# Performance work log

Hardware: AMD Instinct MI355X
Metric: run time of the kernel (lower is better)

## Reference

```python
import jax, jax.numpy as jnp
import numpy as np

N, K, H, W = 2048, 8, 128, 128
G = 50              # glimpse size (50x50 from tem_rnn input 50*50)
ENC = 100           # glimpse encoder output (relation_rnn input arithmetic)
HID = 256
D_REL = ENC + (3 + 50) * 2 + HID          # 462
D_TEM = G * G + (3 + 50) * 2 + HID        # 2862


def _lin(k, out_d, in_d, scale=0.02):
    k1, k2 = jax.random.split(k)
    return (jax.random.normal(k1, (out_d, in_d), jnp.float32) * scale,
            jax.random.normal(k2, (out_d,), jnp.float32) * scale)


def _lstm_params(k, in_d, hid):
    k1, k2, k3, k4 = jax.random.split(k, 4)
    s = 0.02
    return (jax.random.normal(k1, (4 * hid, in_d), jnp.float32) * s,
            jax.random.normal(k2, (4 * hid, hid), jnp.float32) * s,
            jax.random.normal(k3, (4 * hid,), jnp.float32) * s,
            jax.random.normal(k4, (4 * hid,), jnp.float32) * s)


def lstm_cell(x, h, c, Wih, Whh, bih, bhh):
    g = x @ Wih.T + h @ Whh.T + (bih + bhh)
    i, f, gg, o = jnp.split(g, 4, axis=-1)
    i, f, o = jax.nn.sigmoid(i), jax.nn.sigmoid(f), jax.nn.sigmoid(o)
    c2 = f * c + i * jnp.tanh(gg)
    return o * jnp.tanh(c2), c2


def _bilinear_one(im, py, px):
    # im [H,W]; py,px [G,G] pixel coords; zeros padding like torch grid_sample
    x0 = jnp.floor(px); y0 = jnp.floor(py)
    wx1 = px - x0; wy1 = py - y0
    x0i = x0.astype(jnp.int32); y0i = y0.astype(jnp.int32)

    def gather(yi, xi):
        valid = (yi >= 0) & (yi < H) & (xi >= 0) & (xi < W)
        v = im[jnp.clip(yi, 0, H - 1), jnp.clip(xi, 0, W - 1)]
        return jnp.where(valid, v, 0.0)

    return ((1 - wy1) * (1 - wx1) * gather(y0i, x0i)
            + (1 - wy1) * wx1 * gather(y0i, x0i + 1)
            + wy1 * (1 - wx1) * gather(y0i + 1, x0i)
            + wy1 * wx1 * gather(y0i + 1, x0i + 1))


def stn_glimpse(z_where, img):
    # z_where [n,3] = (scale, tx, ty); theta = [[s,0,tx],[0,s,ty]] (attentive_stn_encode)
    s, tx, ty = z_where[:, 0], z_where[:, 1], z_where[:, 2]
    lin = jnp.linspace(-1.0, 1.0, G)
    gy, gx = jnp.meshgrid(lin, lin, indexing='ij')           # [G,G]
    px = (s[:, None, None] * gx + tx[:, None, None] + 1.0) * 0.5 * (W - 1)
    py = (s[:, None, None] * gy + ty[:, None, None] + 1.0) * 0.5 * (H - 1)
    out = jax.vmap(_bilinear_one)(img, py, px)               # [n,G,G]
    return out.reshape(out.shape[0], G * G)


def setup_inputs() -> dict:
    key = jax.random.key(0)
    ks = jax.random.split(key, 16)
    inp = {
        'img': jax.random.uniform(ks[0], (N, H, W), jnp.float32),
        'z_what_last': jax.random.normal(ks[1], (N, K, 50), jnp.float32),
        'z_where_last': jax.random.normal(ks[2], (N, K, 3), jnp.float32) * 0.3,
        'z_pres_last': jnp.ones((N, K, 1), jnp.float32),
        'hidden_last': jax.random.normal(ks[3], (N, K, HID), jnp.float32),
    }
    inp['W_loca'], inp['b_loca'] = _lin(ks[4], 3, HID)
    inp['Wg'], inp['bg'] = _lin(ks[5], ENC, G * G)
    (inp['Wih_rel'], inp['Whh_rel'], inp['bih_rel'], inp['bhh_rel']) = _lstm_params(ks[6], D_REL, HID)
    (inp['Wih_tem'], inp['Whh_tem'], inp['bih_tem'], inp['bhh_tem']) = _lstm_params(ks[7], D_TEM, HID)
    inp['Wm_wh'], inp['bm_wh'] = _lin(ks[8], 3, HID + 3)
    inp['Ws_wh'], inp['bs_wh'] = _lin(ks[9], 3, HID + 3)
    inp['Wm_wt'], inp['bm_wt'] = _lin(ks[10], 50, 50 + HID + HID)
    inp['Ws_wt'], inp['bs_wt'] = _lin(ks[11], 50, 50 + HID + HID)
    inp['Wm_pr'], inp['bm_pr'] = _lin(ks[12], 1, 50 + 3 + HID + HID)
    inp['Ws_pr'], inp['bs_pr'] = _lin(ks[13], 1, 50 + 3 + HID + HID)
    return inp


def reference(img, z_what_last, z_where_last, z_pres_last, hidden_last,
              W_loca, b_loca, Wg, bg,
              Wih_rel, Whh_rel, bih_rel, bhh_rel,
              Wih_tem, Whh_tem, bih_tem, bhh_tem,
              Wm_wh, bm_wh, Ws_wh, bs_wh,
              Wm_wt, bm_wt, Ws_wt, bs_wt,
              Wm_pr, bm_pr, Ws_pr, bs_pr):
    n = img.shape[0]

    def step(carry, xs):
        h_r, c_r, pzw, pzwhat = carry
        zwl, zwhatl, zpl, hl = xs   # [n,3],[n,50],[n,1],[n,256]
        # prop_loca: relu(linear(hidden)) + z_where_last
        zwb = jax.nn.relu(hl @ W_loca.T + b_loca) + zwl
        # STN glimpse + encode (bias pass)
        enc = jax.nn.relu(stn_glimpse(zwb, img) @ Wg.T + bg)        # [n,100]
        rin = jnp.concatenate([enc, zwl, pzw, zwhatl, pzwhat, hl], -1)  # [n,462]
        h_r2, c_r2 = lstm_cell(rin, h_r, c_r, Wih_rel, Whh_rel, bih_rel, bhh_rel)
        # z_where: latent predictor mean (eval mode)
        zw = jnp.concatenate([zwl, h_r2], -1) @ Wm_wh.T + bm_wh      # [n,3]
        # second STN glimpse with sampled where
        g2 = stn_glimpse(zw, img)                                    # [n,2500]
        tin = jnp.concatenate([g2, zw, pzw, zwhatl, pzwhat, hl], -1) # [n,2862]
        h_t, c_t = lstm_cell(tin, h_r2, c_r2, Wih_tem, Whh_tem, bih_tem, bhh_tem)
        # z_what mean
        zwhat = jnp.concatenate([zwhatl, h_r2, h_t], -1) @ Wm_wt.T + bm_wt  # [n,50]
        # z_pres: deterministic expectation of Bernoulli(mean*std) * previous pres
        zp_cal = jnp.concatenate([zwhat, zw, h_r2, h_t], -1)
        p = jax.nn.sigmoid(zp_cal @ Wm_pr.T + bm_pr) * jax.nn.sigmoid(zp_cal @ Ws_pr.T + bs_pr)
        zp = p * zpl                                                 # [n,1]
        return (h_r2, c_r2, zw, zwhat), (zwhat, zw, zp, h_t)

    carry0 = (jnp.zeros((n, HID), img.dtype), jnp.zeros((n, HID), img.dtype),
              jnp.zeros((n, 3), img.dtype), jnp.zeros((n, 50), img.dtype))
    xs = (jnp.swapaxes(z_where_last, 0, 1), jnp.swapaxes(z_what_last, 0, 1),
          jnp.swapaxes(z_pres_last, 0, 1), jnp.swapaxes(hidden_last, 0, 1))
    _, (zwhat_s, zw_s, zp_s, ht_s) = jax.lax.scan(step, carry0, xs)
    z_what = jnp.swapaxes(zwhat_s, 0, 1)   # [n,K,50]
    z_where = jnp.swapaxes(zw_s, 0, 1)     # [n,K,3]
    z_pres = jnp.swapaxes(zp_s, 0, 1)      # [n,K,1]
    h_temp = jnp.swapaxes(ht_s, 0, 1)      # [n,K,256]
    return z_what, z_where, z_pres, h_temp
```

## Files before the change

### kernel.cpp

```cpp
#include <hip/hip_runtime.h>
#include <hip/hip_bf16.h>
#include <math.h>

typedef __attribute__((ext_vector_type(8))) short bf16x8;
typedef __attribute__((ext_vector_type(4))) float f32x4;
using bf16 = __hip_bfloat16;

constexpr int NN   = 2048;
constexpr int KO   = 8;
constexpr int IH   = 128, IW = 128;
constexpr int GS   = 50;
constexpr int HIDD = 256;
constexpr int RIN_LD = 768;
constexpr int TIN_LD = 3136;
constexpr int G1_LD  = 2560;

__device__ __forceinline__ float sigm(float x) { return 1.f/(1.f+expf(-x)); }

template<int OUT_BF16, int RELU>
__global__ __launch_bounds__(256, 4) void mfma_gemm(
    const bf16* __restrict__ A, int lda, int Ktot,
    const bf16* __restrict__ Wt, int ldw, int M,
    const float* __restrict__ b1, const float* __restrict__ b2,
    void* __restrict__ Cout, int ldc, int nxb, int Kseg, int sstride)
{
    __shared__ __align__(16) bf16 As[2*4096];
    __shared__ __align__(16) bf16 Bs[2*4096];
    const int b    = blockIdx.x;
    const int xcd  = b & 7;
    const int t    = b >> 3;
    const int n0   = (xcd + 8*(t / nxb))*64;
    const int m0   = (t % nxb)*64;
    const int tid  = threadIdx.x;
    const int w    = tid>>6, lane = tid&63;
    const int wy   = w>>1, wx = w&1;
    const int q    = lane>>4, fr = lane&15;

    const int kbeg = blockIdx.y * Kseg;
    const int kend = min(Ktot, kbeg + Kseg);
    const int nk   = (kend - kbeg) >> 6;

    const int r0   = tid>>3;
    const int csrc = ((tid&7)*8) ^ ((r0&7)<<3);
    const bf16* pa = A + (size_t)(n0 + r0)*lda + kbeg + csrc;
    int wmr0 = m0 + r0;       if (wmr0 > M-1) wmr0 = M-1;
    int wmr1 = m0 + r0 + 32;  if (wmr1 > M-1) wmr1 = M-1;
    const bf16* pb  = Wt + (size_t)wmr0*ldw + kbeg + csrc;
    const bf16* pb1 = Wt + (size_t)wmr1*ldw + kbeg + csrc;

    f32x4 acc[2][2] = {};

    auto stage = [&](int buf, int koff) {
        bf16* la = As + buf*4096 + w*512;
        bf16* lb = Bs + buf*4096 + w*512;
        __builtin_amdgcn_global_load_lds(
            (const __attribute__((address_space(1))) void*)(pa + koff),
            (__attribute__((address_space(3))) void*)la, 16, 0, 0);
        __builtin_amdgcn_global_load_lds(
            (const __attribute__((address_space(1))) void*)(pa + koff + 32*(size_t)lda),
            (__attribute__((address_space(3))) void*)(la + 2048), 16, 0, 0);
        __builtin_amdgcn_global_load_lds(
            (const __attribute__((address_space(1))) void*)(pb + koff),
            (__attribute__((address_space(3))) void*)lb, 16, 0, 0);
        __builtin_amdgcn_global_load_lds(
            (const __attribute__((address_space(1))) void*)(pb1 + koff),
            (__attribute__((address_space(3))) void*)(lb + 2048), 16, 0, 0);
    };

    stage(0, 0);
    __syncthreads();
    int cur = 0;
    for (int kt = 0; kt < nk; ++kt) {
        if (kt + 1 < nk) stage(cur ^ 1, (kt + 1) << 6);
        const bf16* Ab = As + cur*4096;
        const bf16* Bb = Bs + cur*4096;
        bf16x8 av[2][2], bv[2][2];
        #pragma unroll
        for (int i=0;i<2;i++) {
            int r = wy*32 + i*16 + fr;
            int sw = (r&7)<<3, base = r*64;
            av[i][0] = *(const bf16x8*)(Ab + base + ((q*8) ^ sw));
            av[i][1] = *(const bf16x8*)(Ab + base + ((32 + q*8) ^ sw));
        }
        #pragma unroll
        for (int j=0;j<2;j++) {
            int r = wx*32 + j*16 + fr;
            int sw = (r&7)<<3, base = r*64;
            bv[j][0] = *(const bf16x8*)(Bb + base + ((q*8) ^ sw));
            bv[j][1] = *(const bf16x8*)(Bb + base + ((32 + q*8) ^ sw));
        }
        #pragma unroll
        for (int h=0;h<2;h++)
            #pragma unroll
            for (int i=0;i<2;i++)
                #pragma unroll
                for (int j=0;j<2;j++)
                    acc[i][j] = __builtin_amdgcn_mfma_f32_16x16x32_bf16(av[i][h], bv[j][h], acc[i][j], 0, 0, 0);
        __syncthreads();
        cur ^= 1;
    }

    #pragma unroll
    for (int j=0;j<2;j++) {
        int col = m0 + wx*32 + j*16 + fr;
        if (col < M) {
            float bias = 0.f;
            if (blockIdx.y == 0) {
                if (b1) bias += b1[col];
                if (b2) bias += b2[col];
            }
            #pragma unroll
            for (int i=0;i<2;i++) {
                #pragma unroll
                for (int reg=0;reg<4;reg++) {
                    float v = acc[i][j][reg] + bias;
                    if (RELU) v = fmaxf(v, 0.f);
                    size_t idx = (size_t)(n0 + wy*32 + i*16 + q*4 + reg)*ldc + col;
                    if (OUT_BF16) ((bf16*)Cout)[idx] = __float2bfloat16(v);
                    else          ((float*)Cout)[(size_t)blockIdx.y*sstride + idx] = v;
                }
            }
        }
    }
}

__device__ __forceinline__ void glimpse_points_global(const float* __restrict__ im,
                                                      float s, float tx, float ty,
                                                      bf16* __restrict__ drow) {
    const float GXS = 2.0f/49.0f;
    const float txp = tx + 1.0f, typ = ty + 1.0f;
    for (int p2 = threadIdx.x; p2 < 1250; p2 += 256) {
        int i = p2 / 25, j = (p2 - i*25)*2;
        float gy  = fmaf((float)i, GXS, -1.0f);
        float py  = fmaf(s, gy, typ)*63.5f;
        float y0f = floorf(py); float fy = py - y0f; int y0 = (int)y0f;
        float wy0 = ((unsigned)y0     < 128u) ? (1.f - fy) : 0.f;
        float wy1 = ((unsigned)(y0+1) < 128u) ? fy         : 0.f;
        const float* r0 = im + min(max(y0,  0),127)*IW;
        const float* r1 = im + min(max(y0+1,0),127)*IW;
        float gxa = fmaf((float)j, GXS, -1.0f);
        float pxa = fmaf(s, gxa, txp)*63.5f;
        float xa0f = floorf(pxa); float fa = pxa - xa0f; int xa0 = (int)xa0f;
        float wa0 = ((unsigned)xa0     < 128u) ? (1.f - fa) : 0.f;
        float wa1 = ((unsigned)(xa0+1) < 128u) ? fa         : 0.f;
        int xa0c = min(max(xa0,  0),127), xa1c = min(max(xa0+1,0),127);
        float gxb = fmaf((float)(j+1), GXS, -1.0f);
        float pxb = fmaf(s, gxb, txp)*63.5f;
        float xb0f = floorf(pxb); float fb = pxb - xb0f; int xb0 = (int)xb0f;
        float wb0 = ((unsigned)xb0     < 128u) ? (1.f - fb) : 0.f;
        float wb1 = ((unsigned)(xb0+1) < 128u) ? fb         : 0.f;
        int xb0c = min(max(xb0,  0),127), xb1c = min(max(xb0+1,0),127);

        float va = fmaf(wy1, fmaf(wa0, r1[xa0c], wa1*r1[xa1c]),
                   wy0 *     fmaf(wa0, r0[xa0c], wa1*r0[xa1c]));
        float vb = fmaf(wy1, fmaf(wb0, r1[xb0c], wb1*r1[xb1c]),
                   wy0 *     fmaf(wb0, r0[xb0c], wb1*r0[xb1c]));

        bf16 b0 = __float2bfloat16(va), b1 = __float2bfloat16(vb);
        unsigned short u0, u1;
        __builtin_memcpy(&u0, &b0, 2); __builtin_memcpy(&u1, &b1, 2);
        *(unsigned int*)(drow + i*GS + j) = (unsigned)u0 | ((unsigned)u1 << 16);
    }
}

__device__ __forceinline__ void sample_pair_lds(const float* __restrict__ im_s,
                                                float s, float txp, float typ,
                                                int i, int j, bf16* __restrict__ drow) {
    const float GXS = 2.0f/49.0f;
    float gy  = fmaf((float)i, GXS, -1.0f);
    float py  = fmaf(s, gy, typ)*63.5f;
    float y0f = floorf(py); float fy = py - y0f; int y0 = (int)y0f;
    float wy0 = ((unsigned)y0     < 128u) ? (1.f - fy) : 0.f;
    float wy1 = ((unsigned)(y0+1) < 128u) ? fy         : 0.f;
    const float* r0 = im_s + min(max(y0,  0),127)*IW;
    const float* r1 = im_s + min(max(y0+1,0),127)*IW;
    float gxa = fmaf((float)j, GXS, -1.0f);
    float pxa = fmaf(s, gxa, txp)*63.5f;
    float xa0f = floorf(pxa); float fa = pxa - xa0f; int xa0 = (int)xa0f;
    float wa0 = ((unsigned)xa0     < 128u) ? (1.f - fa) : 0.f;
    float wa1 = ((unsigned)(xa0+1) < 128u) ? fa         : 0.f;
    int xa0c = min(max(xa0,  0),127), xa1c = min(max(xa0+1,0),127);
    float gxb = fmaf((float)(j+1), GXS, -1.0f);
    float pxb = fmaf(s, gxb, txp)*63.5f;
    float xb0f = floorf(pxb); float fb = pxb - xb0f; int xb0 = (int)xb0f;
    float wb0 = ((unsigned)xb0     < 128u) ? (1.f - fb) : 0.f;
    float wb1 = ((unsigned)(xb0+1) < 128u) ? fb         : 0.f;
    int xb0c = min(max(xb0,  0),127), xb1c = min(max(xb0+1,0),127);
    float va = fmaf(wy1, fmaf(wa0, r1[xa0c], wa1*r1[xa1c]),
               wy0 *     fmaf(wa0, r0[xa0c], wa1*r0[xa1c]));
    float vb = fmaf(wy1, fmaf(wb0, r1[xb0c], wb1*r1[xb1c]),
               wy0 *     fmaf(wb0, r0[xb0c], wb1*r0[xb1c]));
    bf16 b0 = __float2bfloat16(va), b1 = __float2bfloat16(vb);
    unsigned short u0, u1;
    __builtin_memcpy(&u0, &b0, 2); __builtin_memcpy(&u1, &b1, 2);
    *(unsigned int*)(drow + i*GS + j) = (unsigned)u0 | ((unsigned)u1 << 16);
}

__global__ __launch_bounds__(512) void glimpse_all(const float* __restrict__ img,
                                                   const float* __restrict__ zwb,
                                                   bf16* __restrict__ dst, int ldd,
                                                   bf16* __restrict__ rin,
                                                   const float* __restrict__ z_where_last,
                                                   const float* __restrict__ z_what_last,
                                                   const float* __restrict__ hidden_last,
                                                   int cbase, int CH) {
    __shared__ float im_s[IH*IW];
    const int n = blockIdx.x;
    const float* im = img + (size_t)n*IH*IW;
    {
        const float4* s4 = (const float4*)im;
        float4* d4 = (float4*)im_s;
        #pragma unroll
        for (int t = threadIdx.x; t < IH*IW/4; t += 512) d4[t] = s4[t];
    }
    __syncthreads();

    const int tot = CH*1250;
    for (int p = threadIdx.x; p < tot; p += 512) {
        int sl = p / 1250, p2 = p - sl*1250;
        int i = p2 / 25, j = (p2 - i*25)*2;
        const float* zr = zwb + (size_t)(sl*NN + n)*3;
        float s = zr[0], txp = zr[1] + 1.0f, typ = zr[2] + 1.0f;
        sample_pair_lds(im_s, s, txp, typ, i, j, dst + (size_t)(sl*NN + n)*ldd);
    }

    const int tot2 = CH*309;
    for (int t = threadIdx.x; t < tot2; t += 512) {
        int sl = t / 309, c = t - sl*309;
        int k = cbase + sl;
        bf16* rrow = rin + (size_t)(sl*NN + n)*RIN_LD;
        float v; int col;
        if (c < 3)       { col = 100 + c;      v = z_where_last[((size_t)n*KO + k)*3 + c]; }
        else if (c < 53) { col = 106 + (c-3);  v = z_what_last[((size_t)n*KO + k)*50 + (c-3)]; }
        else             { col = 206 + (c-53); v = hidden_last[((size_t)n*KO + k)*HIDD + (c-53)]; }
        rrow[col] = __float2bfloat16(v);
    }
}

__global__ __launch_bounds__(256) void rel_glimpse2(
    const float* __restrict__ gates, const float* __restrict__ gates2,
    float* __restrict__ h_r, float* __restrict__ c_r,
    const float* __restrict__ z_where_last,
    const float* __restrict__ Wm_wh, const float* __restrict__ bm_wh,
    float* __restrict__ zw_cur, float* __restrict__ out_zwhere,
    bf16* __restrict__ rin_next, bf16* __restrict__ tin,
    const float* __restrict__ img,
    const float* __restrict__ zw_prev, const float* __restrict__ zwhat_prev,
    const float* __restrict__ z_what_last, const float* __restrict__ hidden_last, int k)
{
    __shared__ float hs[256];
    __shared__ float zws[3];
    int n = blockIdx.x, j = threadIdx.x;
    const float* g  = gates  + (size_t)n*1024;
    const float* g2 = gates2 + (size_t)n*1024;
    float ig = sigm(g[j]       + g2[j]);
    float fg = sigm(g[256+j]   + g2[256+j]);
    float gg = tanhf(g[512+j]  + g2[512+j]);
    float og = sigm(g[768+j]   + g2[768+j]);
    int cidx = n*256 + j;
    float c2 = fg*c_r[cidx] + ig*gg;
    float hv = og*tanhf(c2);
    c_r[cidx] = c2;
    h_r[cidx] = hv;
    hs[j] = hv;
    bf16 hb = __float2bfloat16(hv);
    rin_next[(size_t)n*RIN_LD + 462 + j] = hb;
    bf16* trow = tin + (size_t)n*TIN_LD;
    trow[2862 + j] = hb;
    __syncthreads();
    int w = j >> 6, lane = j & 63;
    if (w < 3) {
        const float* wt = Wm_wh + w*259;
        float sa = 0.f;
        for (int i = lane; i < 256; i += 64) sa = fmaf(hs[i], wt[3+i], sa);
        #pragma unroll
        for (int off = 32; off; off >>= 1) sa += __shfl_down(sa, off);
        if (lane == 0) {
            const float* zwl = z_where_last + ((size_t)n*KO + k)*3;
            float acc = bm_wh[w] + sa;
            for (int i = 0; i < 3; i++) acc = fmaf(zwl[i], wt[i], acc);
            zws[w] = acc;
            zw_cur[n*3+w] = acc;
            out_zwhere[((size_t)n*KO + k)*3 + w] = acc;
            bf16 ab = __float2bfloat16(acc);
            rin_next[(size_t)n*RIN_LD + 103 + w] = ab;
            trow[2500 + w] = ab;
        }
    }
    __syncthreads();
    float s = zws[0], tx = zws[1], ty = zws[2];
    glimpse_points_global(img + (size_t)n*IH*IW, s, tx, ty, trow);
    for (int c = 3 + j; c < 362; c += 256) {
        float v;
        if      (c <   6) v = zw_prev[n*3 + c-3];
        else if (c <  56) v = z_what_last[((size_t)n*KO + k)*50 + c-6];
        else if (c < 106) v = zwhat_prev[n*50 + c-56];
        else              v = hidden_last[((size_t)n*KO + k)*HIDD + c-106];
        trow[2500 + c] = __float2bfloat16(v);
    }
}

__global__ void zero_f32(float* __restrict__ p, int n) {
    int i = blockIdx.x*blockDim.x + threadIdx.x;
    if (i < n) p[i] = 0.f;
}

__global__ void repack_w(const float* __restrict__ s1, int K1,
                         const float* __restrict__ s2, int K2,
                         bf16* __restrict__ dst, int ldd, int M) {
    int gid = blockIdx.x*blockDim.x + threadIdx.x;
    if (gid >= M*ldd) return;
    int m = gid / ldd, c = gid - m*ldd;
    float v = 0.f;
    if (c < K1)           v = s1[(size_t)m*K1 + c];
    else if (c < K1+K2)   v = s2[(size_t)m*K2 + (c-K1)];
    dst[gid] = __float2bfloat16(v);
}

__global__ void transpose_wmwt(const float* __restrict__ W, float* __restrict__ Wt) {
    int gid = blockIdx.x*blockDim.x + threadIdx.x;
    if (gid >= 576*64) return;
    int i = gid >> 6, m = gid & 63;
    Wt[gid] = (m < 50 && i < 562) ? W[(size_t)m*562 + i] : 0.f;
}

__global__ __launch_bounds__(256) void zwb_all_v2(const float* __restrict__ hidden_last,
                                                  const float* __restrict__ z_where_last,
                                                  const float* __restrict__ Wl, const float* __restrict__ bl,
                                                  float* __restrict__ zwb_all) {
    __shared__ float wls[768];
    for (int i = threadIdx.x; i < 768; i += 256) wls[i] = Wl[i];
    __syncthreads();
    int wv = threadIdx.x>>6, lane = threadIdx.x&63;
    int row = blockIdx.x*4 + wv;
    int s = row >> 11, n = row & (NN-1);
    const float* hl = hidden_last + ((size_t)n*KO + s)*HIDD;
    float4 h4 = *(const float4*)(hl + lane*4);
    float s0=0.f, s1=0.f, s2=0.f;
    #pragma unroll
    for (int r4=0;r4<4;r4++) {
        float hv = ((const float*)&h4)[r4];
        int i = lane*4 + r4;
        s0 = fmaf(hv, wls[i],     s0);
        s1 = fmaf(hv, wls[256+i], s1);
        s2 = fmaf(hv, wls[512+i], s2);
    }
    #pragma unroll
    for (int off=32; off; off>>=1) {
        s0 += __shfl_down(s0,off); s1 += __shfl_down(s1,off); s2 += __shfl_down(s2,off);
    }
    if (lane == 0) {
        const float* zwl = z_where_last + ((size_t)n*KO + s)*3;
        zwb_all[row*3+0] = fmaxf(s0+bl[0],0.f) + zwl[0];
        zwb_all[row*3+1] = fmaxf(s1+bl[1],0.f) + zwl[1];
        zwb_all[row*3+2] = fmaxf(s2+bl[2],0.f) + zwl[2];
    }
}

__global__ void zero_rin_carry(bf16* __restrict__ rin0) {
    int gid = blockIdx.x*blockDim.x + threadIdx.x;
    if (gid >= NN*309) return;
    int c = gid % 309, n = gid/309;
    int col = (c < 3) ? 103+c : ((c < 53) ? 156+(c-3) : 462+(c-53));
    rin0[(size_t)n*RIN_LD + col] = __float2bfloat16(0.f);
}

__global__ __launch_bounds__(256) void tem_fused(
    const float* __restrict__ gates, const float* __restrict__ gates2,
    const float* __restrict__ c_r, const float* __restrict__ h_r,
    const float* __restrict__ z_what_last,
    const float* __restrict__ wt_t, const float* __restrict__ bm_wt,
    const float* __restrict__ Wm_pr, const float* __restrict__ bm_pr,
    const float* __restrict__ Ws_pr, const float* __restrict__ bs_pr,
    const float* __restrict__ zw_cur, const float* __restrict__ z_pres_last,
    float* __restrict__ zwhat_cur, float* __restrict__ out_zwhat,
    float* __restrict__ out_htemp, float* __restrict__ out_zpres,
    bf16* __restrict__ rin_next, int k)
{
    __shared__ float L[615];
    __shared__ float part[4][64];
    int n = blockIdx.x, j = threadIdx.x;
    const float* g  = gates  + (size_t)n*1024;
    const float* g2 = gates2 + (size_t)n*1024;
    float ig = sigm(g[j]       + g2[j]);
    float fg = sigm(g[256+j]   + g2[256+j]);
    float gg = tanhf(g[512+j]  + g2[512+j]);
    float og = sigm(g[768+j]   + g2[768+j]);
    float c2 = fg*c_r[n*256+j] + ig*gg;
    float hv = og*tanhf(c2);
    out_htemp[((size_t)n*KO + k)*HIDD + j] = hv;
    L[309+j] = hv;
    L[53+j]  = h_r[n*256+j];
    if (j < 50)      L[j]  = z_what_last[((size_t)n*KO + k)*50 + j];
    else if (j < 53) L[j]  = zw_cur[n*3 + (j-50)];
    __syncthreads();
    {
        int m = j & 63, grp = j >> 6;
        float sa = 0.f;
        for (int i = grp; i < 562; i += 4) {
            float v = (i < 50) ? L[i] : L[i+3];
            sa = fmaf(v, wt_t[i*64 + m], sa);
        }
        part[grp][m] = sa;
    }
    __syncthreads();
    if (j < 50) {
        float acc = part[0][j] + part[1][j] + part[2][j] + part[3][j] + bm_wt[j];
        zwhat_cur[n*50+j] = acc;
        out_zwhat[((size_t)n*KO + k)*50 + j] = acc;
        rin_next[(size_t)n*RIN_LD + 156 + j] = __float2bfloat16(acc);
        L[565+j] = acc;
    }
    __syncthreads();
    if (j < 64) {
        float s1 = 0.f, s2 = 0.f;
        for (int i = j; i < 565; i += 64) {
            float v = (i < 50) ? L[565+i] : L[i];
            s1 = fmaf(v, Wm_pr[i], s1);
            s2 = fmaf(v, Ws_pr[i], s2);
        }
        #pragma unroll
        for (int off = 32; off; off >>= 1) { s1 += __shfl_down(s1,off); s2 += __shfl_down(s2,off); }
        if (j == 0) {
            float p = sigm(s1 + bm_pr[0]) * sigm(s2 + bs_pr[0]);
            out_zpres[(size_t)n*KO + k] = p * z_pres_last[(size_t)n*KO + k];
        }
    }
}

extern "C" void kernel_launch(void* const* d_in, const int* in_sizes, int n_in,
                              void* d_out, int out_size, void* d_ws, size_t ws_size,
                              hipStream_t stream) {
    (void)in_sizes; (void)n_in; (void)out_size;
    const float* img          = (const float*)d_in[0];
    const float* z_what_last  = (const float*)d_in[1];
    const float* z_where_last = (const float*)d_in[2];
    const float* z_pres_last  = (const float*)d_in[3];
    const float* hidden_last  = (const float*)d_in[4];
    const float* W_loca = (const float*)d_in[5];
    const float* b_loca = (const float*)d_in[6];
    const float* Wg     = (const float*)d_in[7];
    const float* bg     = (const float*)d_in[8];
    const float* Wih_rel = (const float*)d_in[9];
    const float* Whh_rel = (const float*)d_in[10];
    const float* bih_rel = (const float*)d_in[11];
    const float* bhh_rel = (const float*)d_in[12];
    const float* Wih_tem = (const float*)d_in[13];
    const float* Whh_tem = (const float*)d_in[14];
    const float* bih_tem = (const float*)d_in[15];
    const float* bhh_tem = (const float*)d_in[16];
    const float* Wm_wh = (const float*)d_in[17];
    const float* bm_wh = (const float*)d_in[18];
    const float* Wm_wt = (const float*)d_in[21];
    const float* bm_wt = (const float*)d_in[22];
    const float* Wm_pr = (const float*)d_in[25];
    const float* bm_pr = (const float*)d_in[26];
    const float* Ws_pr = (const float*)d_in[27];
    const float* bs_pr = (const float*)d_in[28];

    char* base_p = (char*)d_ws;
    size_t off = 0;
    auto carve = [&](size_t bytes) -> char* {
        char* r = base_p + off;
        off += (bytes + 255) & ~(size_t)255;
        return r;
    };
    bf16*  tin      = (bf16*) carve((size_t)NN*TIN_LD*2);
    float* gates    = (float*)carve((size_t)2*NN*1024*4);
    bf16*  W_tem    = (bf16*) carve((size_t)1024*TIN_LD*2);
    bf16*  W_rel    = (bf16*) carve((size_t)1024*RIN_LD*2);
    bf16*  Wg_bf    = (bf16*) carve((size_t)100*G1_LD*2);
    float* wt_t     = (float*)carve((size_t)576*64*4);
    float* zwb_all  = (float*)carve((size_t)KO*NN*3*4);
    float* h_r      = (float*)carve((size_t)NN*HIDD*4);
    float* c_r      = (float*)carve((size_t)NN*HIDD*4);
    float* zw1      = (float*)carve((size_t)NN*3*4);
    float* zwhat1   = (float*)carve((size_t)NN*50*4);
    float* zw0      = (float*)carve((size_t)NN*3*4);
    float* zwhat0   = (float*)carve((size_t)NN*50*4);
    size_t fixed_bytes = off;
    float* gates2 = gates + (size_t)NN*1024;

    int CH = 1;
    for (int cand : {8, 4, 2}) {
        size_t need = fixed_bytes
                    + (((size_t)cand*NN*G1_LD*2 + 255) & ~(size_t)255)
                    + (((size_t)cand*NN*RIN_LD*2 + 255) & ~(size_t)255);
        if (need <= ws_size) { CH = cand; break; }
    }
    bf16* g1 = nullptr; int g1ld;
    bf16* rin;
    if (CH > 1) {
        g1   = (bf16*)carve((size_t)CH*NN*G1_LD*2);
        rin  = (bf16*)carve((size_t)CH*NN*RIN_LD*2);
        g1ld = G1_LD;
    } else {
        rin  = (bf16*)carve((size_t)NN*RIN_LD*2);
        g1   = tin;
        g1ld = TIN_LD;
    }

    float* out        = (float*)d_out;
    float* out_zwhat  = out;
    float* out_zwhere = out + (size_t)NN*KO*50;
    float* out_zpres  = out_zwhere + (size_t)NN*KO*3;
    float* out_htemp  = out_zpres + (size_t)NN*KO;

    {
        int nz = NN*(HIDD + 3 + 50);
        zero_f32<<<(nz+255)/256, 256, 0, stream>>>(c_r, nz);
    }
    zero_rin_carry<<<(NN*309+255)/256, 256, 0, stream>>>(rin);
    repack_w<<<((1024*RIN_LD)+255)/256, 256, 0, stream>>>(Wih_rel, 462, Whh_rel, 256, W_rel, RIN_LD, 1024);
    repack_w<<<((1024*TIN_LD)+255)/256, 256, 0, stream>>>(Wih_tem, 2862, Whh_tem, 256, W_tem, TIN_LD, 1024);
    repack_w<<<((100*G1_LD)+255)/256, 256, 0, stream>>>(Wg, 2500, nullptr, 0, Wg_bf, G1_LD, 100);
    transpose_wmwt<<<(576*64+255)/256, 256, 0, stream>>>(Wm_wt, wt_t);
    zwb_all_v2<<<KO*NN/4, 256, 0, stream>>>(hidden_last, z_where_last, W_loca, b_loca, zwb_all);

    const int GSTR = NN*1024;
    const int KSEG_REL = 384;
    const int KSEG_TEM = 1600;

    for (int cbase = 0; cbase < KO; cbase += CH) {
        glimpse_all<<<NN, 512, 0, stream>>>(img, zwb_all + (size_t)cbase*NN*3, g1, g1ld,
                                            rin, z_where_last, z_what_last, hidden_last, cbase, CH);
        mfma_gemm<1,1><<<dim3(2*CH*32,1), 256, 0, stream>>>(g1, g1ld, G1_LD, Wg_bf, G1_LD, 100,
                                                            bg, nullptr, rin, RIN_LD, 2, G1_LD, 0);

        for (int s = 0; s < CH; ++s) {
            int k = cbase + s;
            bf16* rin_k  = rin + (size_t)s*NN*RIN_LD;
            bf16* rin_nx = rin + (size_t)((s+1)%CH)*NN*RIN_LD;
            float* zw_cur     = (k & 1) ? zw1 : zw0;
            float* zw_prev    = (k & 1) ? zw0 : zw1;
            float* zwhat_cur  = (k & 1) ? zwhat1 : zwhat0;
            float* zwhat_prev = (k & 1) ? zwhat0 : zwhat1;

            mfma_gemm<0,0><<<dim3(512,2), 256, 0, stream>>>(rin_k, RIN_LD, RIN_LD, W_rel, RIN_LD, 1024,
                                                            bih_rel, bhh_rel, gates, 1024, 16, KSEG_REL, GSTR);
            rel_glimpse2<<<NN, 256, 0, stream>>>(gates, gates2, h_r, c_r, z_where_last, Wm_wh, bm_wh,
                                                 zw_cur, out_zwhere, rin_nx, tin,
                                                 img, zw_prev, zwhat_prev, z_what_last, hidden_last, k);
            mfma_gemm<0,0><<<dim3(512,2), 256, 0, stream>>>(tin, TIN_LD, TIN_LD, W_tem, TIN_LD, 1024,
                                                            bih_tem, bhh_tem, gates, 1024, 16, KSEG_TEM, GSTR);
            tem_fused<<<NN, 256, 0, stream>>>(gates, gates2, c_r, h_r, z_what_last, wt_t, bm_wt, Wm_pr, bm_pr, Ws_pr, bs_pr,
                                              zw_cur, z_pres_last, zwhat_cur, out_zwhat, out_htemp, out_zpres, rin_nx, k);
        }
    }
}
```

Before: 1.138 ms.

## Use larger 128-row MFMA GEMM tiles and 4-way split-K for LSTM gate GEMMs

Adds a gemm128 kernel with 128-row tiles and 64 or 128 output columns per block, replacing the 64x64 GEMM for the relation and temporal LSTM gate projections. The temporal GEMM now uses a 4-way K split, and the LSTM cell kernels sum a variable number of partial gate buffers. The gates workspace is enlarged to hold four partials. Larger tiles increase operand reuse per LDS load, but there is no double buffering and occupancy may drop. The extra split adds partial-sum traffic.

```diff
diff --git a/kernel.cpp b/kernel.cpp
--- a/kernel.cpp
+++ b/kernel.cpp
@@ -14,6 +14,7 @@
 constexpr int RIN_LD = 768;
 constexpr int TIN_LD = 3136;
 constexpr int G1_LD  = 2560;
+constexpr int GSTR   = NN*1024;
 
 __device__ __forceinline__ float sigm(float x) { return 1.f/(1.f+expf(-x)); }
 
@@ -121,6 +122,93 @@
                 }
             }
         }
+    }
+}
+
+template<int JT>
+__global__ __launch_bounds__(256, 2) void gemm128(
+    const bf16* __restrict__ A, int lda, int Ktot,
+    const bf16* __restrict__ Wt, int ldw,
+    const float* __restrict__ b1, const float* __restrict__ b2,
+    float* __restrict__ Cout, int ldc, int nxb, int Kseg, int sstride)
+{
+    constexpr int BMC = JT*32;
+    __shared__ __align__(16) bf16 As[128*64];
+    __shared__ __align__(16) bf16 Bs[BMC*64];
+    const int b    = blockIdx.x;
+    const int xcd  = b & 7;
+    const int t    = b >> 3;
+    const int n0   = (xcd + 8*(t / nxb))*128;
+    const int m0   = (t % nxb)*BMC;
+    const int tid  = threadIdx.x;
+    const int w    = tid>>6, lane = tid&63;
+    const int wy   = w>>1, wx = w&1;
+    const int q    = lane>>4, fr = lane&15;
+
+    const int kbeg = blockIdx.y * Kseg;
+    const int kend = min(Ktot, kbeg + Kseg);
+    const int nk   = (kend - kbeg) >> 6;
+
+    const int r0 = tid>>3;
+    const int c0 = (tid&7)*8;
+
+    f32x4 acc[4][JT] = {};
+
+    for (int kt = 0; kt < nk; ++kt) {
+        const int koff = kbeg + (kt<<6);
+        __syncthreads();
+        #pragma unroll
+        for (int p=0;p<4;p++) {
+            int row = p*32 + r0;
+            int csrc = c0 ^ ((row&7)<<3);
+            __builtin_amdgcn_global_load_lds(
+                (const __attribute__((address_space(1))) void*)(A + (size_t)(n0+row)*lda + koff + csrc),
+                (__attribute__((address_space(3))) void*)(As + p*2048 + w*512), 16, 0, 0);
+        }
+        #pragma unroll
+        for (int p=0;p<JT;p++) {
+            int row = p*32 + r0;
+            int csrc = c0 ^ ((row&7)<<3);
+            __builtin_amdgcn_global_load_lds(
+                (const __attribute__((address_space(1))) void*)(Wt + (size_t)(m0+row)*ldw + koff + csrc),
+                (__attribute__((address_space(3))) void*)(Bs + p*2048 + w*512), 16, 0, 0);
+        }
+        __syncthreads();
+        #pragma unroll
+        for (int h=0;h<2;h++) {
+            bf16x8 av[4], bv[JT];
+            #pragma unroll
+            for (int i=0;i<4;i++) {
+                int r = wy*64 + i*16 + fr;
+                av[i] = *(const bf16x8*)(As + r*64 + ((h*32 + q*8) ^ ((r&7)<<3)));
+            }
+            #pragma unroll
+            for (int j=0;j<JT;j++) {
+                int r = wx*(JT*16) + j*16 + fr;
+                bv[j] = *(const bf16x8*)(Bs + r*64 + ((h*32 + q*8) ^ ((r&7)<<3)));
+            }
+            #pragma unroll
+            for (int i=0;i<4;i++)
+                #pragma unroll
+                for (int j=0;j<JT;j++)
+                    acc[i][j] = __builtin_amdgcn_mfma_f32_16x16x32_bf16(av[i], bv[j], acc[i][j], 0, 0, 0);
+        }
+    }
+
+    float* Cb = Cout + (size_t)blockIdx.y*sstride;
+    #pragma unroll
+    for (int j=0;j<JT;j++) {
+        int col = m0 + wx*(JT*16) + j*16 + fr;
+        float bias = 0.f;
+        if (blockIdx.y == 0) {
+            if (b1) bias += b1[col];
+            if (b2) bias += b2[col];
+        }
+        #pragma unroll
+        for (int i=0;i<4;i++)
+            #pragma unroll
+            for (int reg=0;reg<4;reg++)
+                Cb[(size_t)(n0 + wy*64 + i*16 + q*4 + reg)*ldc + col] = acc[i][j][reg] + bias;
     }
 }
 
@@ -238,7 +326,7 @@
 }
 
 __global__ __launch_bounds__(256) void rel_glimpse2(
-    const float* __restrict__ gates, const float* __restrict__ gates2,
+    const float* __restrict__ gates, int nsplit,
     float* __restrict__ h_r, float* __restrict__ c_r,
     const float* __restrict__ z_where_last,
     const float* __restrict__ Wm_wh, const float* __restrict__ bm_wh,
@@ -251,12 +339,12 @@
     __shared__ float hs[256];
     __shared__ float zws[3];
     int n = blockIdx.x, j = threadIdx.x;
-    const float* g  = gates  + (size_t)n*1024;
-    const float* g2 = gates2 + (size_t)n*1024;
-    float ig = sigm(g[j]       + g2[j]);
-    float fg = sigm(g[256+j]   + g2[256+j]);
-    float gg = tanhf(g[512+j]  + g2[512+j]);
-    float og = sigm(g[768+j]   + g2[768+j]);
+    float sI=0.f, sF=0.f, sG=0.f, sO=0.f;
+    for (int p = 0; p < nsplit; ++p) {
+        const float* g = gates + (size_t)p*GSTR + (size_t)n*1024;
+        sI += g[j]; sF += g[256+j]; sG += g[512+j]; sO += g[768+j];
+    }
+    float ig = sigm(sI), fg = sigm(sF), gg = tanhf(sG), og = sigm(sO);
     int cidx = n*256 + j;
     float c2 = fg*c_r[cidx] + ig*gg;
     float hv = og*tanhf(c2);
@@ -366,7 +454,7 @@
 }
 
 __global__ __launch_bounds__(256) void tem_fused(
-    const float* __restrict__ gates, const float* __restrict__ gates2,
+    const float* __restrict__ gates, int nsplit,
     const float* __restrict__ c_r, const float* __restrict__ h_r,
     const float* __restrict__ z_what_last,
     const float* __restrict__ wt_t, const float* __restrict__ bm_wt,
@@ -380,12 +468,12 @@
     __shared__ float L[615];
     __shared__ float part[4][64];
     int n = blockIdx.x, j = threadIdx.x;
-    const float* g  = gates  + (size_t)n*1024;
-    const float* g2 = gates2 + (size_t)n*1024;
-    float ig = sigm(g[j]       + g2[j]);
-    float fg = sigm(g[256+j]   + g2[256+j]);
-    float gg = tanhf(g[512+j]  + g2[512+j]);
-    float og = sigm(g[768+j]   + g2[768+j]);
+    float sI=0.f, sF=0.f, sG=0.f, sO=0.f;
+    for (int p = 0; p < nsplit; ++p) {
+        const float* g = gates + (size_t)p*GSTR + (size_t)n*1024;
+        sI += g[j]; sF += g[256+j]; sG += g[512+j]; sO += g[768+j];
+    }
+    float ig = sigm(sI), fg = sigm(sF), gg = tanhf(sG), og = sigm(sO);
     float c2 = fg*c_r[n*256+j] + ig*gg;
     float hv = og*tanhf(c2);
     out_htemp[((size_t)n*KO + k)*HIDD + j] = hv;
@@ -466,7 +554,7 @@
         return r;
     };
     bf16*  tin      = (bf16*) carve((size_t)NN*TIN_LD*2);
-    float* gates    = (float*)carve((size_t)2*NN*1024*4);
+    float* gates    = (float*)carve((size_t)4*NN*1024*4);
     bf16*  W_tem    = (bf16*) carve((size_t)1024*TIN_LD*2);
     bf16*  W_rel    = (bf16*) carve((size_t)1024*RIN_LD*2);
     bf16*  Wg_bf    = (bf16*) carve((size_t)100*G1_LD*2);
@@ -479,7 +567,6 @@
     float* zw0      = (float*)carve((size_t)NN*3*4);
     float* zwhat0   = (float*)carve((size_t)NN*50*4);
     size_t fixed_bytes = off;
-    float* gates2 = gates + (size_t)NN*1024;
 
     int CH = 1;
     for (int cand : {8, 4, 2}) {
@@ -517,10 +604,6 @@
     transpose_wmwt<<<(576*64+255)/256, 256, 0, stream>>>(Wm_wt, wt_t);
     zwb_all_v2<<<KO*NN/4, 256, 0, stream>>>(hidden_last, z_where_last, W_loca, b_loca, zwb_all);
 
-    const int GSTR = NN*1024;
-    const int KSEG_REL = 384;
-    const int KSEG_TEM = 1600;
-
     for (int cbase = 0; cbase < KO; cbase += CH) {
         glimpse_all<<<NN, 512, 0, stream>>>(img, zwb_all + (size_t)cbase*NN*3, g1, g1ld,
                                             rin, z_where_last, z_what_last, hidden_last, cbase, CH);
@@ -536,14 +619,14 @@
             float* zwhat_cur  = (k & 1) ? zwhat1 : zwhat0;
             float* zwhat_prev = (k & 1) ? zwhat0 : zwhat1;
 
-            mfma_gemm<0,0><<<dim3(512,2), 256, 0, stream>>>(rin_k, RIN_LD, RIN_LD, W_rel, RIN_LD, 1024,
-                                                            bih_rel, bhh_rel, gates, 1024, 16, KSEG_REL, GSTR);
-            rel_glimpse2<<<NN, 256, 0, stream>>>(gates, gates2, h_r, c_r, z_where_last, Wm_wh, bm_wh,
+            gemm128<2><<<dim3(256,2), 256, 0, stream>>>(rin_k, RIN_LD, RIN_LD, W_rel, RIN_LD,
+                                                        bih_rel, bhh_rel, gates, 1024, 16, 384, GSTR);
+            rel_glimpse2<<<NN, 256, 0, stream>>>(gates, 2, h_r, c_r, z_where_last, Wm_wh, bm_wh,
                                                  zw_cur, out_zwhere, rin_nx, tin,
                                                  img, zw_prev, zwhat_prev, z_what_last, hidden_last, k);
-            mfma_gemm<0,0><<<dim3(512,2), 256, 0, stream>>>(tin, TIN_LD, TIN_LD, W_tem, TIN_LD, 1024,
-                                                            bih_tem, bhh_tem, gates, 1024, 16, KSEG_TEM, GSTR);
-            tem_fused<<<NN, 256, 0, stream>>>(gates, gates2, c_r, h_r, z_what_last, wt_t, bm_wt, Wm_pr, bm_pr, Ws_pr, bs_pr,
+            gemm128<4><<<dim3(128,4), 256, 0, stream>>>(tin, TIN_LD, TIN_LD, W_tem, TIN_LD,
+                                                        bih_tem, bhh_tem, gates, 1024, 8, 832, GSTR);
+            tem_fused<<<NN, 256, 0, stream>>>(gates, 4, c_r, h_r, z_what_last, wt_t, bm_wt, Wm_pr, bm_pr, Ws_pr, bs_pr,
                                               zw_cur, z_pres_last, zwhat_cur, out_zwhat, out_htemp, out_zpres, rin_nx, k);
         }
     }
```

Result: no change. 1.135 ms (-0.3%).
